# Optimization experiments

Measured on AMD Instinct MI355X. Metric: run time of the kernel, lower is better.

The kernel has to match this reference:

```python
import jax, jax.numpy as jnp
import numpy as np

N0, N1, N2 = 262144, 65536, 16384   # sampled src nodes, layer-1 targets, layer-2 targets
E1, E2 = 1048576, 262144            # fanout 16 edges per layer
IN_C, HID_C, OUT_C = 128, 256, 64


def sage_conv(x_src, x_dst, src, dst, num_dst, W_l, W_r, b):
    # PyG SAGEConv (mean aggr): out = mean_{j in N(i)} x_src[j] @ W_l^T + b + x_dst @ W_r^T
    msgs = x_src[src]                                   # [E, C] gather
    s = jax.ops.segment_sum(msgs, dst, num_segments=num_dst)
    cnt = jax.ops.segment_sum(jnp.ones((src.shape[0],), x_src.dtype), dst,
                              num_segments=num_dst)
    aggr = s / jnp.maximum(cnt, 1.0)[:, None]           # mean; isolated nodes -> 0
    return aggr @ W_l.T + b + x_dst @ W_r.T


def setup_inputs() -> dict:
    key = jax.random.key(0)
    ks = jax.random.split(key, 9)
    inp = {
        "x": jax.random.normal(ks[0], (N0, IN_C), dtype=jnp.float32),
        "src1": jax.random.randint(ks[1], (E1,), 0, N0, dtype=jnp.int32),
        "dst1": jax.random.randint(ks[2], (E1,), 0, N1, dtype=jnp.int32),
        "src2": jax.random.randint(ks[3], (E2,), 0, N1, dtype=jnp.int32),
        "dst2": jax.random.randint(ks[4], (E2,), 0, N2, dtype=jnp.int32),
        "W1_l": jax.random.normal(ks[5], (HID_C, IN_C), dtype=jnp.float32) * 0.05,
        "W1_r": jax.random.normal(ks[6], (HID_C, IN_C), dtype=jnp.float32) * 0.05,
        "b1": jnp.zeros((HID_C,), dtype=jnp.float32),
        "W2_l": jax.random.normal(ks[7], (OUT_C, HID_C), dtype=jnp.float32) * 0.05,
        "W2_r": jax.random.normal(ks[8], (OUT_C, HID_C), dtype=jnp.float32) * 0.05,
        "b2": jnp.zeros((OUT_C,), dtype=jnp.float32),
    }
    return inp


def reference(x, src1, dst1, src2, dst2, W1_l, W1_r, b1, W2_l, W2_r, b2):
    # layer 1: sources = all N0 nodes, targets = first N1 nodes (x_target = x[:size[1]])
    h = sage_conv(x, x[:N1], src1, dst1, N1, W1_l, W1_r, b1)   # [N1, HID_C]
    h = jax.nn.relu(h)   # dropout is identity in eval mode
    # layer 2: sources = N1 layer-1 outputs, targets = first N2
    h = sage_conv(h, h[:N2], src2, dst2, N2, W2_l, W2_r, b2)   # [N2, OUT_C]
    return jax.nn.log_softmax(h, axis=-1)
```

## Files before the change

kernel.cpp:

```cpp
#include <hip/hip_runtime.h>
#include <cstdint>
#include <cstddef>

#define N0C 262144
#define N1C 65536
#define N2C 16384
#define E1C 1048576
#define E2C 262144

typedef __attribute__((ext_vector_type(8))) short bf16x8;
typedef __attribute__((ext_vector_type(4))) float f32x4;

__device__ __forceinline__ unsigned short f2bf(float f) {
  union { float f; unsigned u; } q; q.f = f;
  unsigned r = q.u + 0x7fffu + ((q.u >> 16) & 1u);
  return (unsigned short)(r >> 16);
}
__device__ __forceinline__ float blo(unsigned u) {
  union { unsigned u; float f; } q; q.u = u << 16; return q.f;
}
__device__ __forceinline__ float bhi(unsigned u) {
  union { unsigned u; float f; } q; q.u = u & 0xffff0000u; return q.f;
}
__device__ __forceinline__ void gl_lds16(const void* g, void* l) {
  __builtin_amdgcn_global_load_lds((const __attribute__((address_space(1))) void*)g,
                                   (__attribute__((address_space(3))) void*)l, 16, 0, 0);
}

__global__ void cvtbf16_kernel(const float4* __restrict__ in, ushort4* __restrict__ out, int n4) {
  int i = blockIdx.x * blockDim.x + threadIdx.x;
  int stride = gridDim.x * blockDim.x;
  for (; i < n4; i += stride) {
    float4 v = in[i];
    ushort4 o;
    o.x = f2bf(v.x); o.y = f2bf(v.y); o.z = f2bf(v.z); o.w = f2bf(v.w);
    out[i] = o;
  }
}

__global__ __launch_bounds__(256) void cvtw_kernel(
    const float4* __restrict__ W1l, const float4* __restrict__ W1r,
    const float4* __restrict__ W2l, const float4* __restrict__ W2r,
    ushort4* __restrict__ W1lb, ushort4* __restrict__ W1rb,
    ushort4* __restrict__ W2lb, ushort4* __restrict__ W2rb,
    int* __restrict__ btail) {
  int y = blockIdx.y;
  int i = blockIdx.x * 256 + threadIdx.x;
  if (y == 4) {
    if (i < 512) btail[i] = 0;
    return;
  }
  const float4* in; ushort4* outp; int n4;
  if (y == 0)      { in = W1l; outp = W1lb; n4 = 8192; }
  else if (y == 1) { in = W1r; outp = W1rb; n4 = 8192; }
  else if (y == 2) { in = W2l; outp = W2lb; n4 = 4096; }
  else             { in = W2r; outp = W2rb; n4 = 4096; }
  if (i < n4) {
    float4 v = in[i];
    ushort4 o;
    o.x = f2bf(v.x); o.y = f2bf(v.y); o.z = f2bf(v.z); o.w = f2bf(v.w);
    outp[i] = o;
  }
}

template<int SHIFT>
__global__ __launch_bounds__(256) void binA_kernel(const int* __restrict__ src,
                                                   const int* __restrict__ dst,
                                                   int* __restrict__ btail,
                                                   uint2* __restrict__ pairbuf) {
  __shared__ int hist[256];
  __shared__ int lofs[256];
  __shared__ int gbase[256];
  __shared__ int sstg[4096];
  __shared__ int dstg[4096];
  int t = threadIdx.x;
  int e0 = blockIdx.x * 4096;
  hist[t] = 0;
  __syncthreads();
  int s_[16], d_[16], rk[16];
#pragma unroll
  for (int k = 0; k < 16; ++k) {
    int e = e0 + k * 256 + t;
    s_[k] = src[e];
    d_[k] = dst[e];
    rk[k] = atomicAdd(&hist[d_[k] >> SHIFT], 1);
  }
  __syncthreads();
  int v = hist[t];
  lofs[t] = v;
  __syncthreads();
  for (int ofs = 1; ofs < 256; ofs <<= 1) {
    int add = (t >= ofs) ? lofs[t - ofs] : 0;
    __syncthreads();
    lofs[t] += add;
    __syncthreads();
  }
  gbase[t] = atomicAdd(&btail[t], v);
  int excl = lofs[t] - v;
  lofs[t] = excl;
  __syncthreads();
#pragma unroll
  for (int k = 0; k < 16; ++k) {
    int p = lofs[d_[k] >> SHIFT] + rk[k];
    sstg[p] = s_[k];
    dstg[p] = d_[k];
  }
  __syncthreads();
  for (int i = t; i < 4096; i += 256) {
    int d = dstg[i];
    int bk = d >> SHIFT;
    int idx = gbase[bk] + (i - lofs[bk]);
    if (idx < 8192)
      pairbuf[(size_t)bk * 8192 + idx] = make_uint2((unsigned)sstg[i], (unsigned)d);
  }
}

__global__ __launch_bounds__(256) void scanB_kernel(const int* __restrict__ btail,
                                                    int* __restrict__ bbase) {
  __shared__ int s[256];
  int L = blockIdx.x;
  int t = threadIdx.x;
  int v = btail[L * 256 + t];
  s[t] = v;
  __syncthreads();
  for (int ofs = 1; ofs < 256; ofs <<= 1) {
    int add = (t >= ofs) ? s[t - ofs] : 0;
    __syncthreads();
    s[t] += add;
    __syncthreads();
  }
  bbase[L * 256 + t] = s[t] - v;
}

template<int DPB>
__global__ __launch_bounds__(256) void binB_kernel(const uint2* __restrict__ pairbuf,
                                                   const int* __restrict__ btail,
                                                   const int* __restrict__ bbase,
                                                   int* __restrict__ off,
                                                   int* __restrict__ cnt,
                                                   int* __restrict__ ssrc) {
  __shared__ int lcnt[256];
  __shared__ int loff[256];
  __shared__ int lcnt2[256];
  __shared__ int stage[8192];
  int b = blockIdx.x;
  int t = threadIdx.x;
  int n = btail[b];
  if (n > 8192) n = 8192;
  int base = bbase[b];
  lcnt[t] = 0;
  lcnt2[t] = 0;
  __syncthreads();
  const uint2* pb = pairbuf + (size_t)b * 8192;
  for (int i = t; i < n; i += 256) {
    uint2 p = pb[i];
    atomicAdd(&lcnt[p.y & (DPB - 1)], 1);
  }
  __syncthreads();
  int v = lcnt[t];
  loff[t] = v;
  __syncthreads();
  for (int ofs = 1; ofs < 256; ofs <<= 1) {
    int add = (t >= ofs) ? loff[t - ofs] : 0;
    __syncthreads();
    loff[t] += add;
    __syncthreads();
  }
  int excl = loff[t] - v;
  loff[t] = excl;
  if (t < DPB) {
    cnt[b * DPB + t] = v;
    off[b * DPB + t] = base + excl;
  }
  __syncthreads();
  for (int i = t; i < n; i += 256) {
    uint2 p = pb[i];
    int dl = p.y & (DPB - 1);
    int r = atomicAdd(&lcnt2[dl], 1);
    stage[loff[dl] + r] = (int)p.x;
  }
  __syncthreads();
  for (int i = t; i < n; i += 256) ssrc[base + i] = stage[i];
}


__global__ __launch_bounds__(256) void agg1_kernel(const ushort* __restrict__ xb,
                                                   const int* __restrict__ ssrc,
                                                   const int* __restrict__ off,
                                                   const int* __restrict__ cnt,
                                                   ushort* __restrict__ aggr) {
  int wid = (blockIdx.x * 256 + threadIdx.x) >> 6;
  int lane = threadIdx.x & 63;
  int grp = lane >> 4;
  int cl = lane & 15;
  int start = __builtin_amdgcn_readfirstlane(off[wid]);
  int n = __builtin_amdgcn_readfirstlane(cnt[wid]);
  float a0 = 0.f, a1 = 0.f, a2 = 0.f, a3 = 0.f, a4 = 0.f, a5 = 0.f, a6 = 0.f, a7 = 0.f;
  int j = 0;
  for (; j + 4 <= n; j += 4) {
    int s = ssrc[start + j + grp];
    uint4 v = *(const uint4*)(xb + (size_t)s * 128 + cl * 8);
    a0 += blo(v.x); a1 += bhi(v.x); a2 += blo(v.y); a3 += bhi(v.y);
    a4 += blo(v.z); a5 += bhi(v.z); a6 += blo(v.w); a7 += bhi(v.w);
  }
  int rem = n - j;
  if (grp < rem) {
    int s = ssrc[start + j + grp];
    uint4 v = *(const uint4*)(xb + (size_t)s * 128 + cl * 8);
    a0 += blo(v.x); a1 += bhi(v.x); a2 += blo(v.y); a3 += bhi(v.y);
    a4 += blo(v.z); a5 += bhi(v.z); a6 += blo(v.w); a7 += bhi(v.w);
  }
#define RED1(x) x += __shfl_xor(x, 16); x += __shfl_xor(x, 32);
  RED1(a0) RED1(a1) RED1(a2) RED1(a3) RED1(a4) RED1(a5) RED1(a6) RED1(a7)
#undef RED1
  if (lane < 16) {
    float inv = (n > 0) ? 1.0f / (float)n : 0.f;
    uint4 o;
    o.x = (unsigned)f2bf(a0 * inv) | ((unsigned)f2bf(a1 * inv) << 16);
    o.y = (unsigned)f2bf(a2 * inv) | ((unsigned)f2bf(a3 * inv) << 16);
    o.z = (unsigned)f2bf(a4 * inv) | ((unsigned)f2bf(a5 * inv) << 16);
    o.w = (unsigned)f2bf(a6 * inv) | ((unsigned)f2bf(a7 * inv) << 16);
    *(uint4*)(aggr + (size_t)wid * 128 + cl * 8) = o;
  }
}

__global__ __launch_bounds__(256) void agg2_kernel(const ushort* __restrict__ h1b,
                                                   const int* __restrict__ ssrc,
                                                   const int* __restrict__ off,
                                                   const int* __restrict__ cnt,
                                                   ushort* __restrict__ aggr) {
  int wid = (blockIdx.x * 256 + threadIdx.x) >> 6;
  int lane = threadIdx.x & 63;
  int grp = lane >> 5;
  int cl = lane & 31;
  int start = __builtin_amdgcn_readfirstlane(off[wid]);
  int n = __builtin_amdgcn_readfirstlane(cnt[wid]);
  float a0 = 0.f, a1 = 0.f, a2 = 0.f, a3 = 0.f, a4 = 0.f, a5 = 0.f, a6 = 0.f, a7 = 0.f;
  int j = 0;
  for (; j + 4 <= n; j += 4) {
    int sa = ssrc[start + j + grp];
    int sb = ssrc[start + j + 2 + grp];
    uint4 va = *(const uint4*)(h1b + (size_t)sa * 256 + cl * 8);
    uint4 vb = *(const uint4*)(h1b + (size_t)sb * 256 + cl * 8);
    a0 += blo(va.x) + blo(vb.x); a1 += bhi(va.x) + bhi(vb.x);
    a2 += blo(va.y) + blo(vb.y); a3 += bhi(va.y) + bhi(vb.y);
    a4 += blo(va.z) + blo(vb.z); a5 += bhi(va.z) + bhi(vb.z);
    a6 += blo(va.w) + blo(vb.w); a7 += bhi(va.w) + bhi(vb.w);
  }
  if (j + 2 <= n) {
    int s = ssrc[start + j + grp];
    uint4 v = *(const uint4*)(h1b + (size_t)s * 256 + cl * 8);
    a0 += blo(v.x); a1 += bhi(v.x); a2 += blo(v.y); a3 += bhi(v.y);
    a4 += blo(v.z); a5 += bhi(v.z); a6 += blo(v.w); a7 += bhi(v.w);
    j += 2;
  }
  if (grp < n - j) {
    int s = ssrc[start + j + grp];
    uint4 v = *(const uint4*)(h1b + (size_t)s * 256 + cl * 8);
    a0 += blo(v.x); a1 += bhi(v.x); a2 += blo(v.y); a3 += bhi(v.y);
    a4 += blo(v.z); a5 += bhi(v.z); a6 += blo(v.w); a7 += bhi(v.w);
  }
#define RED2(x) x += __shfl_xor(x, 32);
  RED2(a0) RED2(a1) RED2(a2) RED2(a3) RED2(a4) RED2(a5) RED2(a6) RED2(a7)
#undef RED2
  if (lane < 32) {
    float inv = (n > 0) ? 1.0f / (float)n : 0.f;
    uint4 o;
    o.x = (unsigned)f2bf(a0 * inv) | ((unsigned)f2bf(a1 * inv) << 16);
    o.y = (unsigned)f2bf(a2 * inv) | ((unsigned)f2bf(a3 * inv) << 16);
    o.z = (unsigned)f2bf(a4 * inv) | ((unsigned)f2bf(a5 * inv) << 16);
    o.w = (unsigned)f2bf(a6 * inv) | ((unsigned)f2bf(a7 * inv) << 16);
    *(uint4*)(aggr + (size_t)wid * 256 + cl * 8) = o;
  }
}

__global__ __launch_bounds__(256) void mgemm1_kernel(
    const ushort* __restrict__ aggr1, const ushort* __restrict__ xb,
    const ushort* __restrict__ W1lb, const ushort* __restrict__ W1rb,
    const float* __restrict__ b1, ushort* __restrict__ h1b) {
  __shared__ ushort smem[2 * 128 * 64];
  ushort* sA = smem;
  ushort* sB = smem + 128 * 64;
  int t = threadIdx.x;
  int lane = t & 63;
  int w = t >> 6;
  int wm = w >> 1, wn = w & 1;
  int i0 = blockIdx.x * 128;
  int c0 = blockIdx.y * 128;

  int sr = t >> 3;
  int sc = (t & 7) ^ (sr & 7);
  int quad = lane >> 4;
  int l15 = lane & 15;
  int xorv = lane & 7;

  f32x4 acc[4][4];
#pragma unroll
  for (int i = 0; i < 4; ++i)
#pragma unroll
    for (int j = 0; j < 4; ++j) acc[i][j] = (f32x4)(0.f);

  for (int kt = 0; kt < 4; ++kt) {
    const ushort* Asrc = (kt < 2) ? aggr1 : xb;
    const ushort* Bsrc = (kt < 2) ? W1lb : W1rb;
    int koff = (kt & 1) * 64;
#pragma unroll
    for (int it = 0; it < 4; ++it) {
      int r = it * 32 + sr;
      gl_lds16(Asrc + (size_t)(i0 + r) * 128 + koff + sc * 8, sA + (it * 256 + t) * 8);
    }
#pragma unroll
    for (int it = 0; it < 4; ++it) {
      int r = it * 32 + sr;
      gl_lds16(Bsrc + (size_t)(c0 + r) * 128 + koff + sc * 8, sB + (it * 256 + t) * 8);
    }
    __syncthreads();
#pragma unroll
    for (int s = 0; s < 2; ++s) {
      int chunk = ((s * 4 + quad) ^ xorv) * 8;
      bf16x8 av[4], bv[4];
#pragma unroll
      for (int fi = 0; fi < 4; ++fi)
        av[fi] = *(const bf16x8*)(sA + (wm * 64 + fi * 16 + l15) * 64 + chunk);
#pragma unroll
      for (int fj = 0; fj < 4; ++fj)
        bv[fj] = *(const bf16x8*)(sB + (wn * 64 + fj * 16 + l15) * 64 + chunk);
#pragma unroll
      for (int fi = 0; fi < 4; ++fi)
#pragma unroll
        for (int fj = 0; fj < 4; ++fj)
          acc[fi][fj] = __builtin_amdgcn_mfma_f32_16x16x32_bf16(av[fi], bv[fj], acc[fi][fj], 0, 0, 0);
    }
    __syncthreads();
  }

  ushort* eb = smem + w * 4096;
#pragma unroll
  for (int fj = 0; fj < 4; ++fj) {
    float bias = b1[c0 + wn * 64 + fj * 16 + l15];
#pragma unroll
    for (int fi = 0; fi < 4; ++fi) {
#pragma unroll
      for (int r = 0; r < 4; ++r) {
        float v = fmaxf(acc[fi][fj][r] + bias, 0.f);
        eb[(fi * 16 + quad * 4 + r) * 64 + fj * 16 + l15] = f2bf(v);
      }
    }
  }
#pragma unroll
  for (int i = 0; i < 16; ++i) {
    int row = i * 4 + (lane >> 4);
    uint2 v = *(const uint2*)(eb + row * 64 + l15 * 4);
    *(uint2*)(h1b + (size_t)(i0 + wm * 64 + row) * 256 + c0 + wn * 64 + l15 * 4) = v;
  }
}

__global__ __launch_bounds__(256) void mgemm2_kernel(
    const ushort* __restrict__ aggr2, const ushort* __restrict__ h1b,
    const ushort* __restrict__ W2lb, const ushort* __restrict__ W2rb,
    const float* __restrict__ b2, float* __restrict__ out) {
  __shared__ ushort sA[64 * 64];
  __shared__ ushort sB[64 * 64];
  int t = threadIdx.x;
  int lane = t & 63;
  int w = t >> 6;
  int i0 = blockIdx.x * 64;

  int sr = t >> 3;
  int sc = (t & 7) ^ (sr & 7);
  int quad = lane >> 4;
  int l15 = lane & 15;
  int xorv = lane & 7;

  f32x4 acc[4];
#pragma unroll
  for (int j = 0; j < 4; ++j) acc[j] = (f32x4)(0.f);

  for (int kt = 0; kt < 8; ++kt) {
    const ushort* Asrc = (kt < 4) ? aggr2 : h1b;
    const ushort* Bsrc = (kt < 4) ? W2lb : W2rb;
    int koff = (kt & 3) * 64;
#pragma unroll
    for (int it = 0; it < 2; ++it) {
      int r = it * 32 + sr;
      gl_lds16(Asrc + (size_t)(i0 + r) * 256 + koff + sc * 8, sA + (it * 256 + t) * 8);
    }
#pragma unroll
    for (int it = 0; it < 2; ++it) {
      int r = it * 32 + sr;
      gl_lds16(Bsrc + (size_t)r * 256 + koff + sc * 8, sB + (it * 256 + t) * 8);
    }
    __syncthreads();
#pragma unroll
    for (int s = 0; s < 2; ++s) {
      int chunk = ((s * 4 + quad) ^ xorv) * 8;
      bf16x8 av = *(const bf16x8*)(sA + (w * 16 + l15) * 64 + chunk);
      bf16x8 bv[4];
#pragma unroll
      for (int fj = 0; fj < 4; ++fj)
        bv[fj] = *(const bf16x8*)(sB + (fj * 16 + l15) * 64 + chunk);
#pragma unroll
      for (int fj = 0; fj < 4; ++fj)
        acc[fj] = __builtin_amdgcn_mfma_f32_16x16x32_bf16(av, bv[fj], acc[fj], 0, 0, 0);
    }
    __syncthreads();
  }

  float b2c[4];
#pragma unroll
  for (int fj = 0; fj < 4; ++fj) b2c[fj] = b2[fj * 16 + l15];

#pragma unroll
  for (int r = 0; r < 4; ++r) {
    int row = i0 + w * 16 + quad * 4 + r;
    float v[4];
#pragma unroll
    for (int fj = 0; fj < 4; ++fj) v[fj] = acc[fj][r] + b2c[fj];
    float m = fmaxf(fmaxf(v[0], v[1]), fmaxf(v[2], v[3]));
    m = fmaxf(m, __shfl_xor(m, 1));
    m = fmaxf(m, __shfl_xor(m, 2));
    m = fmaxf(m, __shfl_xor(m, 4));
    m = fmaxf(m, __shfl_xor(m, 8));
    float ssum = __expf(v[0] - m) + __expf(v[1] - m) + __expf(v[2] - m) + __expf(v[3] - m);
    ssum += __shfl_xor(ssum, 1);
    ssum += __shfl_xor(ssum, 2);
    ssum += __shfl_xor(ssum, 4);
    ssum += __shfl_xor(ssum, 8);
    float lg = m + __logf(ssum);
#pragma unroll
    for (int fj = 0; fj < 4; ++fj)
      out[(size_t)row * 64 + fj * 16 + l15] = v[fj] - lg;
  }
}


extern "C" void kernel_launch(void* const* d_in, const int* in_sizes, int n_in,
                              void* d_out, int out_size, void* d_ws, size_t ws_size,
                              hipStream_t stream) {
  const float* x   = (const float*)d_in[0];
  const int* src1  = (const int*)d_in[1];
  const int* dst1  = (const int*)d_in[2];
  const int* src2  = (const int*)d_in[3];
  const int* dst2  = (const int*)d_in[4];
  const float* W1l = (const float*)d_in[5];
  const float* W1r = (const float*)d_in[6];
  const float* b1  = (const float*)d_in[7];
  const float* W2l = (const float*)d_in[8];
  const float* W2r = (const float*)d_in[9];
  const float* b2  = (const float*)d_in[10];
  float* out = (float*)d_out;

  char* base = (char*)d_ws;
  ushort* xb   = (ushort*)base;
  ushort* h1b  = (ushort*)(base + 67108864);
  ushort* ag1b = (ushort*)(base + 100663296);
  uint2* pair1 = (uint2*)(base + 117440512);
  uint2* pair2 = (uint2*)(base + 134217728);
  int* cnt1  = (int*)(base + 150994944);
  int* off1  = cnt1 + N1C;
  int* cnt2  = off1 + N1C;
  int* off2  = cnt2 + N2C;
  int* btail = off2 + N2C;
  int* bbase = btail + 512;
  int* ssrc1 = bbase + 512;
  int* ssrc2 = ssrc1 + E1C;
  ushort* W1lb = (ushort*)(ssrc2 + E2C);
  ushort* W1rb = W1lb + 32768;
  ushort* W2lb = W1rb + 32768;
  ushort* W2rb = W2lb + 16384;
  ushort* ag2b = xb;

  cvtw_kernel<<<dim3(32, 5), 256, 0, stream>>>(
      (const float4*)W1l, (const float4*)W1r, (const float4*)W2l, (const float4*)W2r,
      (ushort4*)W1lb, (ushort4*)W1rb, (ushort4*)W2lb, (ushort4*)W2rb, btail);

  cvtbf16_kernel<<<4096, 256, 0, stream>>>((const float4*)x, (ushort4*)xb, N0C * 128 / 4);

  binA_kernel<8><<<E1C / 4096, 256, 0, stream>>>(src1, dst1, btail, pair1);
  binA_kernel<6><<<E2C / 4096, 256, 0, stream>>>(src2, dst2, btail + 256, pair2);
  scanB_kernel<<<2, 256, 0, stream>>>(btail, bbase);
  binB_kernel<256><<<256, 256, 0, stream>>>(pair1, btail, bbase, off1, cnt1, ssrc1);
  binB_kernel<64><<<256, 256, 0, stream>>>(pair2, btail + 256, bbase + 256, off2, cnt2, ssrc2);

  agg1_kernel<<<N1C / 4, 256, 0, stream>>>(xb, ssrc1, off1, cnt1, ag1b);
  mgemm1_kernel<<<dim3(N1C / 128, 2), 256, 0, stream>>>(ag1b, xb, W1lb, W1rb, b1, h1b);

  agg2_kernel<<<N2C / 4, 256, 0, stream>>>(h1b, ssrc2, off2, cnt2, ag2b);
  mgemm2_kernel<<<N2C / 64, 256, 0, stream>>>(ag2b, h1b, W2lb, W2rb, b2, out);
}
```

Before: 184.1 us.

## Drop full x bf16 conversion, merge binning launches, widen layer-1 GEMM tile

Removes the bf16 conversion pass over all of x. Layer-1 aggregation now gathers fp32 rows directly, and only the first N1 rows of x are converted to bf16 inside agg1 for the root-weight GEMM. The two binA launches and the two binB launches are each merged into one grid, and the bucket-base scan is folded into binB as a per-block prefix reduction, so scanB is gone. mgemm1 now uses 512-thread blocks covering all 256 output columns, so the A tile is loaded once instead of twice, at the cost of doubling gather bytes in agg1 and extra LDS and serialised epilogue phases.

```diff
diff --git a/kernel.cpp b/kernel.cpp
--- a/kernel.cpp
+++ b/kernel.cpp
@@ -25,17 +25,6 @@
 __device__ __forceinline__ void gl_lds16(const void* g, void* l) {
   __builtin_amdgcn_global_load_lds((const __attribute__((address_space(1))) void*)g,
                                    (__attribute__((address_space(3))) void*)l, 16, 0, 0);
-}
-
-__global__ void cvtbf16_kernel(const float4* __restrict__ in, ushort4* __restrict__ out, int n4) {
-  int i = blockIdx.x * blockDim.x + threadIdx.x;
-  int stride = gridDim.x * blockDim.x;
-  for (; i < n4; i += stride) {
-    float4 v = in[i];
-    ushort4 o;
-    o.x = f2bf(v.x); o.y = f2bf(v.y); o.z = f2bf(v.z); o.w = f2bf(v.w);
-    out[i] = o;
-  }
 }
 
 __global__ __launch_bounds__(256) void cvtw_kernel(
@@ -63,18 +52,20 @@
   }
 }
 
-template<int SHIFT>
-__global__ __launch_bounds__(256) void binA_kernel(const int* __restrict__ src,
-                                                   const int* __restrict__ dst,
-                                                   int* __restrict__ btail,
-                                                   uint2* __restrict__ pairbuf) {
+__global__ __launch_bounds__(256) void binA_kernel(
+    const int* __restrict__ src1, const int* __restrict__ dst1,
+    const int* __restrict__ src2, const int* __restrict__ dst2,
+    int* __restrict__ btail, uint2* __restrict__ pair1, uint2* __restrict__ pair2) {
   __shared__ int hist[256];
   __shared__ int lofs[256];
   __shared__ int gbase[256];
   __shared__ int sstg[4096];
   __shared__ int dstg[4096];
+  int b = blockIdx.x;
   int t = threadIdx.x;
-  int e0 = blockIdx.x * 4096;
+  const int* src; const int* dst; int shift; int* bt; uint2* pb; int e0;
+  if (b < 256) { src = src1; dst = dst1; shift = 8; bt = btail;       pb = pair1; e0 = b * 4096; }
+  else         { src = src2; dst = dst2; shift = 6; bt = btail + 256; pb = pair2; e0 = (b - 256) * 4096; }
   hist[t] = 0;
   __syncthreads();
   int s_[16], d_[16], rk[16];
@@ -83,7 +74,7 @@
     int e = e0 + k * 256 + t;
     s_[k] = src[e];
     d_[k] = dst[e];
-    rk[k] = atomicAdd(&hist[d_[k] >> SHIFT], 1);
+    rk[k] = atomicAdd(&hist[d_[k] >> shift], 1);
   }
   __syncthreads();
   int v = hist[t];
@@ -95,66 +86,56 @@
     lofs[t] += add;
     __syncthreads();
   }
-  gbase[t] = atomicAdd(&btail[t], v);
+  gbase[t] = atomicAdd(&bt[t], v);
   int excl = lofs[t] - v;
   lofs[t] = excl;
   __syncthreads();
 #pragma unroll
   for (int k = 0; k < 16; ++k) {
-    int p = lofs[d_[k] >> SHIFT] + rk[k];
+    int p = lofs[d_[k] >> shift] + rk[k];
     sstg[p] = s_[k];
     dstg[p] = d_[k];
   }
   __syncthreads();
   for (int i = t; i < 4096; i += 256) {
     int d = dstg[i];
-    int bk = d >> SHIFT;
+    int bk = d >> shift;
     int idx = gbase[bk] + (i - lofs[bk]);
     if (idx < 8192)
-      pairbuf[(size_t)bk * 8192 + idx] = make_uint2((unsigned)sstg[i], (unsigned)d);
-  }
-}
-
-__global__ __launch_bounds__(256) void scanB_kernel(const int* __restrict__ btail,
-                                                    int* __restrict__ bbase) {
-  __shared__ int s[256];
-  int L = blockIdx.x;
-  int t = threadIdx.x;
-  int v = btail[L * 256 + t];
-  s[t] = v;
-  __syncthreads();
-  for (int ofs = 1; ofs < 256; ofs <<= 1) {
-    int add = (t >= ofs) ? s[t - ofs] : 0;
-    __syncthreads();
-    s[t] += add;
-    __syncthreads();
-  }
-  bbase[L * 256 + t] = s[t] - v;
-}
-
-template<int DPB>
-__global__ __launch_bounds__(256) void binB_kernel(const uint2* __restrict__ pairbuf,
-                                                   const int* __restrict__ btail,
-                                                   const int* __restrict__ bbase,
-                                                   int* __restrict__ off,
-                                                   int* __restrict__ cnt,
-                                                   int* __restrict__ ssrc) {
+      pb[(size_t)bk * 8192 + idx] = make_uint2((unsigned)sstg[i], (unsigned)d);
+  }
+}
+
+__global__ __launch_bounds__(256) void binB_kernel(
+    const uint2* __restrict__ pair1, const uint2* __restrict__ pair2,
+    const int* __restrict__ btail,
+    int* __restrict__ off1, int* __restrict__ cnt1, int* __restrict__ ssrc1,
+    int* __restrict__ off2, int* __restrict__ cnt2, int* __restrict__ ssrc2) {
   __shared__ int lcnt[256];
   __shared__ int loff[256];
   __shared__ int lcnt2[256];
   __shared__ int stage[8192];
   int b = blockIdx.x;
   int t = threadIdx.x;
-  int n = btail[b];
-  if (n > 8192) n = 8192;
-  int base = bbase[b];
+  const uint2* pb; const int* bt; int dpb; int* off; int* cnt; int* ssrc; int bl;
+  if (b < 256) { bl = b;       pb = pair1 + (size_t)bl * 8192; bt = btail;       dpb = 256; off = off1; cnt = cnt1; ssrc = ssrc1; }
+  else         { bl = b - 256; pb = pair2 + (size_t)bl * 8192; bt = btail + 256; dpb = 64;  off = off2; cnt = cnt2; ssrc = ssrc2; }
+  lcnt[t] = (t < bl) ? bt[t] : 0;
+  __syncthreads();
+  for (int ofs = 128; ofs > 0; ofs >>= 1) {
+    if (t < ofs) lcnt[t] += lcnt[t + ofs];
+    __syncthreads();
+  }
+  int base = lcnt[0];
+  __syncthreads();
   lcnt[t] = 0;
   lcnt2[t] = 0;
   __syncthreads();
-  const uint2* pb = pairbuf + (size_t)b * 8192;
+  int n = bt[bl];
+  if (n > 8192) n = 8192;
   for (int i = t; i < n; i += 256) {
     uint2 p = pb[i];
-    atomicAdd(&lcnt[p.y & (DPB - 1)], 1);
+    atomicAdd(&lcnt[p.y & (dpb - 1)], 1);
   }
   __syncthreads();
   int v = lcnt[t];
@@ -168,14 +149,14 @@
   }
   int excl = loff[t] - v;
   loff[t] = excl;
-  if (t < DPB) {
-    cnt[b * DPB + t] = v;
-    off[b * DPB + t] = base + excl;
+  if (t < dpb) {
+    cnt[bl * dpb + t] = v;
+    off[bl * dpb + t] = base + excl;
   }
   __syncthreads();
   for (int i = t; i < n; i += 256) {
     uint2 p = pb[i];
-    int dl = p.y & (DPB - 1);
+    int dl = p.y & (dpb - 1);
     int r = atomicAdd(&lcnt2[dl], 1);
     stage[loff[dl] + r] = (int)p.x;
   }
@@ -183,14 +164,19 @@
   for (int i = t; i < n; i += 256) ssrc[base + i] = stage[i];
 }
 
-
-__global__ __launch_bounds__(256) void agg1_kernel(const ushort* __restrict__ xb,
+__global__ __launch_bounds__(256) void agg1_kernel(const float* __restrict__ x,
                                                    const int* __restrict__ ssrc,
                                                    const int* __restrict__ off,
                                                    const int* __restrict__ cnt,
-                                                   ushort* __restrict__ aggr) {
+                                                   ushort* __restrict__ aggr,
+                                                   ushort* __restrict__ xbd) {
   int wid = (blockIdx.x * 256 + threadIdx.x) >> 6;
   int lane = threadIdx.x & 63;
+  {
+    float2 v = ((const float2*)(x + (size_t)wid * 128))[lane];
+    unsigned o = (unsigned)f2bf(v.x) | ((unsigned)f2bf(v.y) << 16);
+    *(unsigned*)(xbd + (size_t)wid * 128 + lane * 2) = o;
+  }
   int grp = lane >> 4;
   int cl = lane & 15;
   int start = __builtin_amdgcn_readfirstlane(off[wid]);
@@ -199,18 +185,21 @@
   int j = 0;
   for (; j + 4 <= n; j += 4) {
     int s = ssrc[start + j + grp];
-    uint4 v = *(const uint4*)(xb + (size_t)s * 128 + cl * 8);
-    a0 += blo(v.x); a1 += bhi(v.x); a2 += blo(v.y); a3 += bhi(v.y);
-    a4 += blo(v.z); a5 += bhi(v.z); a6 += blo(v.w); a7 += bhi(v.w);
-  }
-  int rem = n - j;
-  if (grp < rem) {
+    const float4* row = (const float4*)(x + (size_t)s * 128);
+    float4 va = row[cl * 2];
+    float4 vb = row[cl * 2 + 1];
+    a0 += va.x; a1 += va.y; a2 += va.z; a3 += va.w;
+    a4 += vb.x; a5 += vb.y; a6 += vb.z; a7 += vb.w;
+  }
+  if (grp < n - j) {
     int s = ssrc[start + j + grp];
-    uint4 v = *(const uint4*)(xb + (size_t)s * 128 + cl * 8);
-    a0 += blo(v.x); a1 += bhi(v.x); a2 += blo(v.y); a3 += bhi(v.y);
-    a4 += blo(v.z); a5 += bhi(v.z); a6 += blo(v.w); a7 += bhi(v.w);
-  }
-#define RED1(x) x += __shfl_xor(x, 16); x += __shfl_xor(x, 32);
+    const float4* row = (const float4*)(x + (size_t)s * 128);
+    float4 va = row[cl * 2];
+    float4 vb = row[cl * 2 + 1];
+    a0 += va.x; a1 += va.y; a2 += va.z; a3 += va.w;
+    a4 += vb.x; a5 += vb.y; a6 += vb.z; a7 += vb.w;
+  }
+#define RED1(v) v += __shfl_xor(v, 16); v += __shfl_xor(v, 32);
   RED1(a0) RED1(a1) RED1(a2) RED1(a3) RED1(a4) RED1(a5) RED1(a6) RED1(a7)
 #undef RED1
   if (lane < 16) {
@@ -260,7 +249,7 @@
     a0 += blo(v.x); a1 += bhi(v.x); a2 += blo(v.y); a3 += bhi(v.y);
     a4 += blo(v.z); a5 += bhi(v.z); a6 += blo(v.w); a7 += bhi(v.w);
   }
-#define RED2(x) x += __shfl_xor(x, 32);
+#define RED2(v) v += __shfl_xor(v, 32);
   RED2(a0) RED2(a1) RED2(a2) RED2(a3) RED2(a4) RED2(a5) RED2(a6) RED2(a7)
 #undef RED2
   if (lane < 32) {
@@ -274,19 +263,18 @@
   }
 }
 
-__global__ __launch_bounds__(256) void mgemm1_kernel(
-    const ushort* __restrict__ aggr1, const ushort* __restrict__ xb,
+__global__ __launch_bounds__(512) void mgemm1_kernel(
+    const ushort* __restrict__ aggr1, const ushort* __restrict__ xbd,
     const ushort* __restrict__ W1lb, const ushort* __restrict__ W1rb,
     const float* __restrict__ b1, ushort* __restrict__ h1b) {
-  __shared__ ushort smem[2 * 128 * 64];
+  __shared__ ushort smem[24576];
   ushort* sA = smem;
-  ushort* sB = smem + 128 * 64;
+  ushort* sB = smem + 8192;
   int t = threadIdx.x;
   int lane = t & 63;
   int w = t >> 6;
-  int wm = w >> 1, wn = w & 1;
+  int wm = w >> 2, wn = w & 3;
   int i0 = blockIdx.x * 128;
-  int c0 = blockIdx.y * 128;
 
   int sr = t >> 3;
   int sc = (t & 7) ^ (sr & 7);
@@ -301,18 +289,18 @@
     for (int j = 0; j < 4; ++j) acc[i][j] = (f32x4)(0.f);
 
   for (int kt = 0; kt < 4; ++kt) {
-    const ushort* Asrc = (kt < 2) ? aggr1 : xb;
+    const ushort* Asrc = (kt < 2) ? aggr1 : xbd;
     const ushort* Bsrc = (kt < 2) ? W1lb : W1rb;
     int koff = (kt & 1) * 64;
 #pragma unroll
+    for (int it = 0; it < 2; ++it) {
+      int r = it * 64 + sr;
+      gl_lds16(Asrc + (size_t)(i0 + r) * 128 + koff + sc * 8, sA + (it * 512 + t) * 8);
+    }
+#pragma unroll
     for (int it = 0; it < 4; ++it) {
-      int r = it * 32 + sr;
-      gl_lds16(Asrc + (size_t)(i0 + r) * 128 + koff + sc * 8, sA + (it * 256 + t) * 8);
-    }
-#pragma unroll
-    for (int it = 0; it < 4; ++it) {
-      int r = it * 32 + sr;
-      gl_lds16(Bsrc + (size_t)(c0 + r) * 128 + koff + sc * 8, sB + (it * 256 + t) * 8);
+      int r = it * 64 + sr;
+      gl_lds16(Bsrc + (size_t)r * 128 + koff + sc * 8, sB + (it * 512 + t) * 8);
     }
     __syncthreads();
 #pragma unroll
@@ -334,24 +322,28 @@
     __syncthreads();
   }
 
-  ushort* eb = smem + w * 4096;
-#pragma unroll
-  for (int fj = 0; fj < 4; ++fj) {
-    float bias = b1[c0 + wn * 64 + fj * 16 + l15];
-#pragma unroll
-    for (int fi = 0; fi < 4; ++fi) {
-#pragma unroll
-      for (int r = 0; r < 4; ++r) {
-        float v = fmaxf(acc[fi][fj][r] + bias, 0.f);
-        eb[(fi * 16 + quad * 4 + r) * 64 + fj * 16 + l15] = f2bf(v);
+  for (int ph = 0; ph < 2; ++ph) {
+    if (wm == ph) {
+      ushort* eb = smem + (w & 3) * 4096;
+#pragma unroll
+      for (int fj = 0; fj < 4; ++fj) {
+        float bias = b1[wn * 64 + fj * 16 + l15];
+#pragma unroll
+        for (int fi = 0; fi < 4; ++fi)
+#pragma unroll
+          for (int r = 0; r < 4; ++r) {
+            float v = fmaxf(acc[fi][fj][r] + bias, 0.f);
+            eb[(fi * 16 + quad * 4 + r) * 64 + fj * 16 + l15] = f2bf(v);
+          }
       }
-    }
-  }
-#pragma unroll
-  for (int i = 0; i < 16; ++i) {
-    int row = i * 4 + (lane >> 4);
-    uint2 v = *(const uint2*)(eb + row * 64 + l15 * 4);
-    *(uint2*)(h1b + (size_t)(i0 + wm * 64 + row) * 256 + c0 + wn * 64 + l15 * 4) = v;
+#pragma unroll
+      for (int i = 0; i < 16; ++i) {
+        int row = i * 4 + (lane >> 4);
+        uint2 v = *(const uint2*)(eb + row * 64 + l15 * 4);
+        *(uint2*)(h1b + (size_t)(i0 + wm * 64 + row) * 256 + wn * 64 + l15 * 4) = v;
+      }
+    }
+    __syncthreads();
   }
 }
 
@@ -451,39 +443,34 @@
   float* out = (float*)d_out;
 
   char* base = (char*)d_ws;
-  ushort* xb   = (ushort*)base;
-  ushort* h1b  = (ushort*)(base + 67108864);
-  ushort* ag1b = (ushort*)(base + 100663296);
-  uint2* pair1 = (uint2*)(base + 117440512);
-  uint2* pair2 = (uint2*)(base + 134217728);
-  int* cnt1  = (int*)(base + 150994944);
+  ushort* ag1b = (ushort*)base;
+  ushort* xbd  = (ushort*)(base + 16777216);
+  ushort* h1b  = (ushort*)(base + 33554432);
+  ushort* ag2b = (ushort*)(base + 67108864);
+  uint2* pair1 = (uint2*)(base + 75497472);
+  uint2* pair2 = (uint2*)(base + 92274688);
+  int* cnt1  = (int*)(base + 109051904);
   int* off1  = cnt1 + N1C;
   int* cnt2  = off1 + N1C;
   int* off2  = cnt2 + N2C;
   int* btail = off2 + N2C;
-  int* bbase = btail + 512;
-  int* ssrc1 = bbase + 512;
+  int* ssrc1 = btail + 512;
   int* ssrc2 = ssrc1 + E1C;
   ushort* W1lb = (ushort*)(ssrc2 + E2C);
   ushort* W1rb = W1lb + 32768;
   ushort* W2lb = W1rb + 32768;
   ushort* W2rb = W2lb + 16384;
-  ushort* ag2b = xb;
 
   cvtw_kernel<<<dim3(32, 5), 256, 0, stream>>>(
       (const float4*)W1l, (const float4*)W1r, (const float4*)W2l, (const float4*)W2r,
       (ushort4*)W1lb, (ushort4*)W1rb, (ushort4*)W2lb, (ushort4*)W2rb, btail);
 
-  cvtbf16_kernel<<<4096, 256, 0, stream>>>((const float4*)x, (ushort4*)xb, N0C * 128 / 4);
-
-  binA_kernel<8><<<E1C / 4096, 256, 0, stream>>>(src1, dst1, btail, pair1);
-  binA_kernel<6><<<E2C / 4096, 256, 0, stream>>>(src2, dst2, btail + 256, pair2);
-  scanB_kernel<<<2, 256, 0, stream>>>(btail, bbase);
-  binB_kernel<256><<<256, 256, 0, stream>>>(pair1, btail, bbase, off1, cnt1, ssrc1);
-  binB_kernel<64><<<256, 256, 0, stream>>>(pair2, btail + 256, bbase + 256, off2, cnt2, ssrc2);
-
-  agg1_kernel<<<N1C / 4, 256, 0, stream>>>(xb, ssrc1, off1, cnt1, ag1b);
-  mgemm1_kernel<<<dim3(N1C / 128, 2), 256, 0, stream>>>(ag1b, xb, W1lb, W1rb, b1, h1b);
+  binA_kernel<<<320, 256, 0, stream>>>(src1, dst1, src2, dst2, btail, pair1, pair2);
+  binB_kernel<<<512, 256, 0, stream>>>(pair1, pair2, btail,
+                                       off1, cnt1, ssrc1, off2, cnt2, ssrc2);
+
+  agg1_kernel<<<N1C / 4, 256, 0, stream>>>(x, ssrc1, off1, cnt1, ag1b, xbd);
+  mgemm1_kernel<<<N1C / 128, 512, 0, stream>>>(ag1b, xbd, W1lb, W1rb, b1, h1b);
 
   agg2_kernel<<<N2C / 4, 256, 0, stream>>>(h1b, ssrc2, off2, cnt2, ag2b);
   mgemm2_kernel<<<N2C / 64, 256, 0, stream>>>(ag2b, h1b, W2lb, W2rb, b2, out);
```

Result: faster. 171.5 us (-6.8%).
